# Optimization experiments

Hardware: AMD Instinct MI355X
Metric: run time of the kernel (lower is better)

The kernel has to match this reference:

```python
import jax, jax.numpy as jnp
import numpy as np

N_NODES = 260000          # 10,000 graphs * 26 nodes/graph (split size hardcoded in Net)
N_EDGES = 8320000         # avg degree 32
GRAPH_NODES = 26
IN_DIM, H1, H2 = 4, 26, 11
POOL_OUT = 4              # MaxPool1d(3, stride=3, padding=1) on 11 channels -> 4


def setup_inputs() -> dict:
    key = jax.random.key(0)
    ks = jax.random.split(key, 8)
    x = jax.random.normal(ks[0], (N_NODES, IN_DIM), dtype=jnp.float32)
    edge_index = jax.random.randint(ks[1], (2, N_EDGES), 0, N_NODES, dtype=jnp.int32)
    W1 = jax.random.normal(ks[2], (H1, IN_DIM), dtype=jnp.float32) * 0.3
    b1 = jax.random.normal(ks[3], (H1,), dtype=jnp.float32) * 0.1
    W2 = jax.random.normal(ks[4], (H2, H1), dtype=jnp.float32) * 0.2
    b2 = jax.random.normal(ks[5], (H2,), dtype=jnp.float32) * 0.1
    Wl = jax.random.normal(ks[6], (2, POOL_OUT), dtype=jnp.float32) * 0.3
    bl = jax.random.normal(ks[7], (2,), dtype=jnp.float32) * 0.1
    return {"x": x, "edge_index": edge_index, "W1": W1, "b1": b1,
            "W2": W2, "b2": b2, "Wl": Wl, "bl": bl}


def reference(x, edge_index, W1, b1, W2, b2, Wl, bl):
    N = x.shape[0]
    # add_self_loops
    loops = jnp.arange(N, dtype=edge_index.dtype)
    row = jnp.concatenate([edge_index[0], loops])
    col = jnp.concatenate([edge_index[1], loops])

    def gcn(h, W, b):
        h = h @ W.T + b                       # Linear
        # message: deg = ones -> norm = 1, so message is just x_j = h[row]
        # aggr='add': scatter-add into target nodes (col)
        return jax.ops.segment_sum(h[row], col, num_segments=N)

    h = jnp.tanh(gcn(x, W1, b1))              # [N, 26]
    h = jnp.tanh(gcn(h, W2, b2))              # [N, 11]

    # MaxPool1d(kernel=3, stride=3, padding=1) over the 11 channels -> 4.
    # Left pad by 1 with -inf; the right pad element is never inside a window.
    neg = jnp.full((N, 1), -jnp.inf, dtype=h.dtype)
    hp = jnp.concatenate([neg, h], axis=1)    # [N, 12]
    pooled = hp.reshape(N, POOL_OUT, 3).max(axis=2)  # [N, 4]

    # graph pooling: sum every consecutive block of 26 nodes
    g = pooled.reshape(-1, GRAPH_NODES, POOL_OUT).sum(axis=1)  # [G, 4]

    out = g @ Wl.T + bl                        # [G, 2]
    return jax.nn.softmax(out, axis=-1)        # F.softmax default dim=1 for 2D
```

## Files before the change

kernel.cpp:

```cpp
#include <hip/hip_runtime.h>

#define N_NODES 260000
#define N_EDGES 8320000
#define H1 26
#define H2 11
#define GRAPH_NODES 26
#define N_GRAPHS 10000

#define NB 512
#define NBUCK 508
#define NPB 1024
#define EPB 8125
#define ZSTRIDE 12

__global__ __launch_bounds__(256) void zero_kernel(unsigned* __restrict__ ghist,
                                                   float* __restrict__ gpool) {
    int i = blockIdx.x * 256 + threadIdx.x;
    if (i < 512) ghist[i] = 0u;
    if (i < N_GRAPHS * 4) gpool[i] = 0.f;
}

__global__ __launch_bounds__(256) void count_kernel(const int* __restrict__ col,
                                                    unsigned* __restrict__ ghist) {
    __shared__ unsigned lh[NBUCK];
    for (int b = threadIdx.x; b < NBUCK; b += 256) lh[b] = 0u;
    __syncthreads();
    int stride = gridDim.x * blockDim.x;
    for (int e = blockIdx.x * blockDim.x + threadIdx.x; e < N_EDGES; e += stride)
        atomicAdd(&lh[((unsigned)col[e]) >> 9], 1u);
    __syncthreads();
    for (int b = threadIdx.x; b < NBUCK; b += 256)
        if (lh[b]) atomicAdd(&ghist[b], lh[b]);
}

__global__ __launch_bounds__(512) void scan_kernel(const unsigned* __restrict__ ghist,
                                                   unsigned* __restrict__ bstart,
                                                   unsigned* __restrict__ bfill) {
    __shared__ unsigned v[512];
    int t = threadIdx.x;
    v[t] = (t < NBUCK) ? ghist[t] : 0u;
    __syncthreads();
    for (int off = 1; off < 512; off <<= 1) {
        unsigned add = (t >= off) ? v[t - off] : 0u;
        __syncthreads();
        v[t] += add;
        __syncthreads();
    }
    if (t < NBUCK) {
        unsigned st = (t == 0) ? 0u : v[t - 1];
        bstart[t] = st;
        bfill[t]  = st;
        if (t == NBUCK - 1) bstart[NBUCK] = v[t];
    }
}

__global__ __launch_bounds__(256) void place_kernel(const int* __restrict__ row,
                                                    const int* __restrict__ col,
                                                    unsigned* __restrict__ bfill,
                                                    unsigned* __restrict__ part) {
    __shared__ unsigned lh[NBUCK];
    __shared__ unsigned lbase[NBUCK];
    for (int b = threadIdx.x; b < NBUCK; b += 256) lh[b] = 0u;
    __syncthreads();
    int e0 = blockIdx.x * EPB;
    int e1 = e0 + EPB;
    for (int e = e0 + threadIdx.x; e < e1; e += 256)
        atomicAdd(&lh[((unsigned)col[e]) >> 9], 1u);
    __syncthreads();
    for (int b = threadIdx.x; b < NBUCK; b += 256) {
        unsigned c = lh[b];
        lbase[b] = c ? atomicAdd(&bfill[b], c) : 0u;
    }
    __syncthreads();
    for (int b = threadIdx.x; b < NBUCK; b += 256) lh[b] = 0u;
    __syncthreads();
    for (int e = e0 + threadIdx.x; e < e1; e += 256) {
        unsigned c = (unsigned)col[e];
        unsigned b = c >> 9;
        unsigned p = lbase[b] + atomicAdd(&lh[b], 1u);
        part[p] = (((unsigned)row[e]) << 9) | (c & 511u);
    }
}

__global__ __launch_bounds__(256) void layer1_kernel(const unsigned* __restrict__ part,
                                                     const unsigned* __restrict__ bstart,
                                                     const float* __restrict__ x,
                                                     const float* __restrict__ W1,
                                                     const float* __restrict__ b1,
                                                     const float* __restrict__ W2,
                                                     const float* __restrict__ b2,
                                                     float* __restrict__ zbuf) {
    __shared__ float acc[NB][5];
    __shared__ float sW1[H1 * 4], sb1[H1], sW2[H2 * H1];
    for (int t = threadIdx.x; t < H1 * 4; t += 256) sW1[t] = W1[t];
    for (int t = threadIdx.x; t < H1; t += 256) sb1[t] = b1[t];
    for (int t = threadIdx.x; t < H2 * H1; t += 256) sW2[t] = W2[t];
    for (int t = threadIdx.x; t < NB * 5; t += 256) ((float*)acc)[t] = 0.f;
    __syncthreads();
    unsigned s = bstart[blockIdx.x], e = bstart[blockIdx.x + 1];
    for (unsigned i = s + threadIdx.x; i < e; i += 256) {
        unsigned u = part[i];
        unsigned r = u >> 9, cl = u & 511u;
        float4 xv = ((const float4*)x)[r];
        atomicAdd(&acc[cl][0], xv.x);
        atomicAdd(&acc[cl][1], xv.y);
        atomicAdd(&acc[cl][2], xv.z);
        atomicAdd(&acc[cl][3], xv.w);
        atomicAdd(&acc[cl][4], 1.f);
    }
    __syncthreads();
    int base = blockIdx.x * NB;
    for (int n = threadIdx.x; n < NB; n += 256) {
        int node = base + n;
        if (node >= N_NODES) continue;
        float4 xv = ((const float4*)x)[node];
        float sx = acc[n][0] + xv.x, sy = acc[n][1] + xv.y;
        float sz = acc[n][2] + xv.z, sw = acc[n][3] + xv.w;
        float deg = acc[n][4] + 1.f;
        float h[H1];
        #pragma unroll
        for (int j = 0; j < H1; ++j)
            h[j] = tanhf(sb1[j] * deg + sx * sW1[j*4+0] + sy * sW1[j*4+1]
                                      + sz * sW1[j*4+2] + sw * sW1[j*4+3]);
        float* zp = zbuf + (size_t)node * ZSTRIDE;
        #pragma unroll
        for (int jj = 0; jj < H2; ++jj) {
            float v = 0.f;
            #pragma unroll
            for (int k = 0; k < H1; ++k) v += h[k] * sW2[jj*H1 + k];
            zp[jj] = v;
        }
        zp[H2] = deg;
    }
}

__global__ __launch_bounds__(256) void layer2_kernel(const unsigned* __restrict__ part,
                                                     const unsigned* __restrict__ bstart,
                                                     const float* __restrict__ zbuf,
                                                     const float* __restrict__ b2,
                                                     float* __restrict__ gpool) {
    __shared__ float facc[NB][ZSTRIDE];
    __shared__ float sb2[H2];
    __shared__ float gacc[22][4];
    if (threadIdx.x < H2) sb2[threadIdx.x] = b2[threadIdx.x];
    if (threadIdx.x < 88) ((float*)gacc)[threadIdx.x] = 0.f;
    const float* zslice = zbuf + (size_t)blockIdx.x * NB * ZSTRIDE;
    for (int t = threadIdx.x; t < NB * ZSTRIDE; t += 256)
        ((float*)facc)[t] = zslice[t];
    __syncthreads();
    for (int t = threadIdx.x; t < NB * ZSTRIDE; t += 256) {
        int n = t / ZSTRIDE, ch = t - n * ZSTRIDE;
        if (ch < H2) facc[n][ch] += facc[n][H2] * sb2[ch];
    }
    __syncthreads();
    unsigned s = bstart[blockIdx.x], e = bstart[blockIdx.x + 1];
    int ch = threadIdx.x & 15;
    int sub = threadIdx.x >> 4;
    for (unsigned i = s + sub; i < e; i += 16) {
        unsigned u = part[i];
        unsigned r = u >> 9, cl = u & 511u;
        if (ch < H2) atomicAdd(&facc[cl][ch], zbuf[(size_t)r * ZSTRIDE + ch]);
    }
    __syncthreads();
    int base = blockIdx.x * NB;
    int gfirst = base / GRAPH_NODES;
    int lastnode = min(base + NB - 1, N_NODES - 1);
    int glast = lastnode / GRAPH_NODES;
    for (int n = threadIdx.x; n < NB; n += 256) {
        int node = base + n;
        if (node >= N_NODES) continue;
        const float* h = facc[n];
        float p0 = tanhf(fmaxf(h[0], h[1]));
        float p1 = tanhf(fmaxf(fmaxf(h[2], h[3]), h[4]));
        float p2 = tanhf(fmaxf(fmaxf(h[5], h[6]), h[7]));
        float p3 = tanhf(fmaxf(fmaxf(h[8], h[9]), h[10]));
        int lg = node / GRAPH_NODES - gfirst;
        atomicAdd(&gacc[lg][0], p0);
        atomicAdd(&gacc[lg][1], p1);
        atomicAdd(&gacc[lg][2], p2);
        atomicAdd(&gacc[lg][3], p3);
    }
    __syncthreads();
    int ng = glast - gfirst + 1;
    for (int t = threadIdx.x; t < ng * 4; t += 256) {
        int lg = t >> 2, c = t & 3;
        float v = gacc[lg][c];
        if (v != 0.f) atomicAdd(&gpool[(size_t)(gfirst + lg) * 4 + c], v);
    }
}

__global__ __launch_bounds__(256) void final_kernel(const float* __restrict__ gpool,
                                                    const float* __restrict__ Wl,
                                                    const float* __restrict__ bl,
                                                    float* __restrict__ out) {
    int g = blockIdx.x * 256 + threadIdx.x;
    if (g >= N_GRAPHS) return;
    float4 p = ((const float4*)gpool)[g];
    float o0 = bl[0] + p.x * Wl[0] + p.y * Wl[1] + p.z * Wl[2] + p.w * Wl[3];
    float o1 = bl[1] + p.x * Wl[4] + p.y * Wl[5] + p.z * Wl[6] + p.w * Wl[7];
    float m = fmaxf(o0, o1);
    float e0 = expf(o0 - m), e1 = expf(o1 - m);
    float s = e0 + e1;
    out[g * 2 + 0] = e0 / s;
    out[g * 2 + 1] = e1 / s;
}

extern "C" void kernel_launch(void* const* d_in, const int* in_sizes, int n_in,
                              void* d_out, int out_size, void* d_ws, size_t ws_size,
                              hipStream_t stream) {
    const float* x  = (const float*)d_in[0];
    const int* ei   = (const int*)d_in[1];
    const float* W1 = (const float*)d_in[2];
    const float* b1 = (const float*)d_in[3];
    const float* W2 = (const float*)d_in[4];
    const float* b2 = (const float*)d_in[5];
    const float* Wl = (const float*)d_in[6];
    const float* bl = (const float*)d_in[7];
    float* out = (float*)d_out;

    const int* row = ei;
    const int* col = ei + N_EDGES;

    float*    ws     = (float*)d_ws;
    float*    zbuf   = ws;
    unsigned* part   = (unsigned*)(ws + (size_t)NBUCK * NB * ZSTRIDE);
    unsigned* bstart = part + N_EDGES;
    unsigned* bfill  = bstart + 512;
    unsigned* ghist  = bfill + 512;
    float*    gpool  = (float*)(ghist + 512);

    zero_kernel<<<(N_GRAPHS*4 + 255)/256, 256, 0, stream>>>(ghist, gpool);
    count_kernel<<<NPB, 256, 0, stream>>>(col, ghist);
    scan_kernel<<<1, 512, 0, stream>>>(ghist, bstart, bfill);
    place_kernel<<<NPB, 256, 0, stream>>>(row, col, bfill, part);
    layer1_kernel<<<NBUCK, 256, 0, stream>>>(part, bstart, x, W1, b1, W2, b2, zbuf);
    layer2_kernel<<<NBUCK, 256, 0, stream>>>(part, bstart, zbuf, b2, gpool);
    final_kernel<<<(N_GRAPHS + 255)/256, 256, 0, stream>>>(gpool, Wl, bl, out);
}
```

Before: 1.154 ms.

## Shrink node buckets to 128, vectorize layer2 edge gathers, pad shared stride

Buckets now cover 128 destination nodes instead of 512, so there are four times as many blocks (2032) for the layer kernels and the scan grows to 2048 entries. Layer2 switches from 16 lanes per edge to one thread per edge, loading the 11-channel message as three float4 reads. The shared accumulator stride becomes 13 to reduce bank conflicts. This raises parallelism and cuts wasted lanes, at the cost of more global histogram atomics and more per-thread LDS atomics.

New measurement: 1.072 ms. 7.1% less time.

```diff
diff --git a/kernel.cpp b/kernel.cpp
--- a/kernel.cpp
+++ b/kernel.cpp
@@ -7,16 +7,17 @@
 #define GRAPH_NODES 26
 #define N_GRAPHS 10000
 
-#define NB 512
-#define NBUCK 508
+#define NB 128
+#define NBUCK 2032
 #define NPB 1024
 #define EPB 8125
 #define ZSTRIDE 12
+#define FSTRIDE 13
 
 __global__ __launch_bounds__(256) void zero_kernel(unsigned* __restrict__ ghist,
                                                    float* __restrict__ gpool) {
     int i = blockIdx.x * 256 + threadIdx.x;
-    if (i < 512) ghist[i] = 0u;
+    if (i < NBUCK) ghist[i] = 0u;
     if (i < N_GRAPHS * 4) gpool[i] = 0.f;
 }
 
@@ -27,30 +28,37 @@
     __syncthreads();
     int stride = gridDim.x * blockDim.x;
     for (int e = blockIdx.x * blockDim.x + threadIdx.x; e < N_EDGES; e += stride)
-        atomicAdd(&lh[((unsigned)col[e]) >> 9], 1u);
+        atomicAdd(&lh[((unsigned)col[e]) >> 7], 1u);
     __syncthreads();
     for (int b = threadIdx.x; b < NBUCK; b += 256)
         if (lh[b]) atomicAdd(&ghist[b], lh[b]);
 }
 
-__global__ __launch_bounds__(512) void scan_kernel(const unsigned* __restrict__ ghist,
-                                                   unsigned* __restrict__ bstart,
-                                                   unsigned* __restrict__ bfill) {
-    __shared__ unsigned v[512];
+__global__ __launch_bounds__(1024) void scan_kernel(const unsigned* __restrict__ ghist,
+                                                    unsigned* __restrict__ bstart,
+                                                    unsigned* __restrict__ bfill) {
+    __shared__ unsigned v[2048];
     int t = threadIdx.x;
-    v[t] = (t < NBUCK) ? ghist[t] : 0u;
-    __syncthreads();
-    for (int off = 1; off < 512; off <<= 1) {
-        unsigned add = (t >= off) ? v[t - off] : 0u;
+    int t1 = t + 1024;
+    v[t]  = (t  < NBUCK) ? ghist[t]  : 0u;
+    v[t1] = (t1 < NBUCK) ? ghist[t1] : 0u;
+    __syncthreads();
+    for (int off = 1; off < 2048; off <<= 1) {
+        unsigned a0 = (t  >= off) ? v[t  - off] : 0u;
+        unsigned a1 = (t1 >= off) ? v[t1 - off] : 0u;
         __syncthreads();
-        v[t] += add;
+        v[t]  += a0;
+        v[t1] += a1;
         __syncthreads();
     }
     if (t < NBUCK) {
         unsigned st = (t == 0) ? 0u : v[t - 1];
-        bstart[t] = st;
-        bfill[t]  = st;
-        if (t == NBUCK - 1) bstart[NBUCK] = v[t];
+        bstart[t] = st; bfill[t] = st;
+    }
+    if (t1 < NBUCK) {
+        unsigned st = v[t1 - 1];
+        bstart[t1] = st; bfill[t1] = st;
+        if (t1 == NBUCK - 1) bstart[NBUCK] = v[t1];
     }
 }
 
@@ -65,7 +73,7 @@
     int e0 = blockIdx.x * EPB;
     int e1 = e0 + EPB;
     for (int e = e0 + threadIdx.x; e < e1; e += 256)
-        atomicAdd(&lh[((unsigned)col[e]) >> 9], 1u);
+        atomicAdd(&lh[((unsigned)col[e]) >> 7], 1u);
     __syncthreads();
     for (int b = threadIdx.x; b < NBUCK; b += 256) {
         unsigned c = lh[b];
@@ -76,9 +84,9 @@
     __syncthreads();
     for (int e = e0 + threadIdx.x; e < e1; e += 256) {
         unsigned c = (unsigned)col[e];
-        unsigned b = c >> 9;
+        unsigned b = c >> 7;
         unsigned p = lbase[b] + atomicAdd(&lh[b], 1u);
-        part[p] = (((unsigned)row[e]) << 9) | (c & 511u);
+        part[p] = (((unsigned)row[e]) << 7) | (c & 127u);
     }
 }
 
@@ -89,24 +97,24 @@
                                                      const float* __restrict__ b1,
                                                      const float* __restrict__ W2,
                                                      const float* __restrict__ b2,
-                                                     float* __restrict__ zbuf) {
-    __shared__ float acc[NB][5];
+                                                     float* __restrict__ zmsg) {
+    __shared__ float acc[NB * 5];
     __shared__ float sW1[H1 * 4], sb1[H1], sW2[H2 * H1];
     for (int t = threadIdx.x; t < H1 * 4; t += 256) sW1[t] = W1[t];
     for (int t = threadIdx.x; t < H1; t += 256) sb1[t] = b1[t];
     for (int t = threadIdx.x; t < H2 * H1; t += 256) sW2[t] = W2[t];
-    for (int t = threadIdx.x; t < NB * 5; t += 256) ((float*)acc)[t] = 0.f;
+    for (int t = threadIdx.x; t < NB * 5; t += 256) acc[t] = 0.f;
     __syncthreads();
     unsigned s = bstart[blockIdx.x], e = bstart[blockIdx.x + 1];
     for (unsigned i = s + threadIdx.x; i < e; i += 256) {
         unsigned u = part[i];
-        unsigned r = u >> 9, cl = u & 511u;
+        unsigned r = u >> 7, cl = u & 127u;
         float4 xv = ((const float4*)x)[r];
-        atomicAdd(&acc[cl][0], xv.x);
-        atomicAdd(&acc[cl][1], xv.y);
-        atomicAdd(&acc[cl][2], xv.z);
-        atomicAdd(&acc[cl][3], xv.w);
-        atomicAdd(&acc[cl][4], 1.f);
+        atomicAdd(&acc[cl*5+0], xv.x);
+        atomicAdd(&acc[cl*5+1], xv.y);
+        atomicAdd(&acc[cl*5+2], xv.z);
+        atomicAdd(&acc[cl*5+3], xv.w);
+        atomicAdd(&acc[cl*5+4], 1.f);
     }
     __syncthreads();
     int base = blockIdx.x * NB;
@@ -114,15 +122,15 @@
         int node = base + n;
         if (node >= N_NODES) continue;
         float4 xv = ((const float4*)x)[node];
-        float sx = acc[n][0] + xv.x, sy = acc[n][1] + xv.y;
-        float sz = acc[n][2] + xv.z, sw = acc[n][3] + xv.w;
-        float deg = acc[n][4] + 1.f;
+        float sx = acc[n*5+0] + xv.x, sy = acc[n*5+1] + xv.y;
+        float sz = acc[n*5+2] + xv.z, sw = acc[n*5+3] + xv.w;
+        float deg = acc[n*5+4] + 1.f;
         float h[H1];
         #pragma unroll
         for (int j = 0; j < H1; ++j)
             h[j] = tanhf(sb1[j] * deg + sx * sW1[j*4+0] + sy * sW1[j*4+1]
                                       + sz * sW1[j*4+2] + sw * sW1[j*4+3]);
-        float* zp = zbuf + (size_t)node * ZSTRIDE;
+        float* zp = zmsg + (size_t)node * ZSTRIDE;
         #pragma unroll
         for (int jj = 0; jj < H2; ++jj) {
             float v = 0.f;
@@ -136,30 +144,38 @@
 
 __global__ __launch_bounds__(256) void layer2_kernel(const unsigned* __restrict__ part,
                                                      const unsigned* __restrict__ bstart,
-                                                     const float* __restrict__ zbuf,
+                                                     const float* __restrict__ zmsg,
                                                      const float* __restrict__ b2,
                                                      float* __restrict__ gpool) {
-    __shared__ float facc[NB][ZSTRIDE];
+    __shared__ float facc[NB * FSTRIDE];
     __shared__ float sb2[H2];
-    __shared__ float gacc[22][4];
+    __shared__ float gacc[7][4];
     if (threadIdx.x < H2) sb2[threadIdx.x] = b2[threadIdx.x];
-    if (threadIdx.x < 88) ((float*)gacc)[threadIdx.x] = 0.f;
-    const float* zslice = zbuf + (size_t)blockIdx.x * NB * ZSTRIDE;
-    for (int t = threadIdx.x; t < NB * ZSTRIDE; t += 256)
-        ((float*)facc)[t] = zslice[t];
-    __syncthreads();
+    if (threadIdx.x < 28) ((float*)gacc)[threadIdx.x] = 0.f;
+    const float* zslice = zmsg + (size_t)blockIdx.x * NB * ZSTRIDE;
     for (int t = threadIdx.x; t < NB * ZSTRIDE; t += 256) {
         int n = t / ZSTRIDE, ch = t - n * ZSTRIDE;
-        if (ch < H2) facc[n][ch] += facc[n][H2] * sb2[ch];
+        facc[n * FSTRIDE + ch] = zslice[t];
+    }
+    __syncthreads();
+    for (int t = threadIdx.x; t < NB * H2; t += 256) {
+        int n = t / H2, ch = t - n * H2;
+        facc[n * FSTRIDE + ch] += facc[n * FSTRIDE + H2] * sb2[ch];
     }
     __syncthreads();
     unsigned s = bstart[blockIdx.x], e = bstart[blockIdx.x + 1];
-    int ch = threadIdx.x & 15;
-    int sub = threadIdx.x >> 4;
-    for (unsigned i = s + sub; i < e; i += 16) {
+    for (unsigned i = s + threadIdx.x; i < e; i += 256) {
         unsigned u = part[i];
-        unsigned r = u >> 9, cl = u & 511u;
-        if (ch < H2) atomicAdd(&facc[cl][ch], zbuf[(size_t)r * ZSTRIDE + ch]);
+        unsigned r = u >> 7, cl = u & 127u;
+        const float4* z4 = (const float4*)(zmsg + (size_t)r * ZSTRIDE);
+        float4 a = z4[0], b = z4[1], c = z4[2];
+        float* f = facc + cl * FSTRIDE;
+        atomicAdd(&f[0],  a.x); atomicAdd(&f[1],  a.y);
+        atomicAdd(&f[2],  a.z); atomicAdd(&f[3],  a.w);
+        atomicAdd(&f[4],  b.x); atomicAdd(&f[5],  b.y);
+        atomicAdd(&f[6],  b.z); atomicAdd(&f[7],  b.w);
+        atomicAdd(&f[8],  c.x); atomicAdd(&f[9],  c.y);
+        atomicAdd(&f[10], c.z);
     }
     __syncthreads();
     int base = blockIdx.x * NB;
@@ -169,7 +185,7 @@
     for (int n = threadIdx.x; n < NB; n += 256) {
         int node = base + n;
         if (node >= N_NODES) continue;
-        const float* h = facc[n];
+        const float* h = facc + n * FSTRIDE;
         float p0 = tanhf(fmaxf(h[0], h[1]));
         float p1 = tanhf(fmaxf(fmaxf(h[2], h[3]), h[4]));
         float p2 = tanhf(fmaxf(fmaxf(h[5], h[6]), h[7]));
@@ -222,18 +238,18 @@
     const int* col = ei + N_EDGES;
 
     float*    ws     = (float*)d_ws;
-    float*    zbuf   = ws;
-    unsigned* part   = (unsigned*)(ws + (size_t)NBUCK * NB * ZSTRIDE);
+    float*    zmsg   = ws;
+    unsigned* part   = (unsigned*)(ws + (size_t)(NBUCK * NB) * ZSTRIDE);
     unsigned* bstart = part + N_EDGES;
-    unsigned* bfill  = bstart + 512;
-    unsigned* ghist  = bfill + 512;
-    float*    gpool  = (float*)(ghist + 512);
+    unsigned* bfill  = bstart + NBUCK + 1;
+    unsigned* ghist  = bfill + NBUCK;
+    float*    gpool  = (float*)(ghist + NBUCK);
 
     zero_kernel<<<(N_GRAPHS*4 + 255)/256, 256, 0, stream>>>(ghist, gpool);
     count_kernel<<<NPB, 256, 0, stream>>>(col, ghist);
-    scan_kernel<<<1, 512, 0, stream>>>(ghist, bstart, bfill);
+    scan_kernel<<<1, 1024, 0, stream>>>(ghist, bstart, bfill);
     place_kernel<<<NPB, 256, 0, stream>>>(row, col, bfill, part);
-    layer1_kernel<<<NBUCK, 256, 0, stream>>>(part, bstart, x, W1, b1, W2, b2, zbuf);
-    layer2_kernel<<<NBUCK, 256, 0, stream>>>(part, bstart, zbuf, b2, gpool);
+    layer1_kernel<<<NBUCK, 256, 0, stream>>>(part, bstart, x, W1, b1, W2, b2, zmsg);
+    layer2_kernel<<<NBUCK, 256, 0, stream>>>(part, bstart, zmsg, b2, gpool);
     final_kernel<<<(N_GRAPHS + 255)/256, 256, 0, stream>>>(gpool, Wl, bl, out);
 }
```
